# Performance work log

Hardware: AMD Instinct MI355X
Metric: run time of the kernel (lower is better)

Reference implementation:

```python
import jax, jax.numpy as jnp
import numpy as np
import math

T, B, I, H = 512, 64, 256, 512


def setup_inputs() -> dict:
    key = jax.random.key(0)
    ks = jax.random.split(key, 8)
    inp = {}
    inp["x"] = jax.random.normal(ks[0], (T, B, I), jnp.float32)
    # positive elapsed-time intervals per step/batch
    inp["time"] = jax.random.uniform(ks[1], (T, B), jnp.float32, 0.0, 2.0)
    def wn(k, shape, fan_in):
        return jax.random.normal(k, shape, jnp.float32) * (1.0 / math.sqrt(fan_in))
    # forward-direction cell params
    inp["W_ih_f"] = wn(ks[2], (I, 4 * H), I)
    inp["W_hh_f"] = wn(ks[3], (H, 4 * H), H)
    inp["b_f"] = jnp.zeros((4 * H,), jnp.float32)
    inp["W_d_f"] = wn(ks[4], (H, H), H)
    inp["b_d_f"] = jnp.zeros((H,), jnp.float32)
    # backward-direction cell params
    inp["W_ih_b"] = wn(ks[5], (I, 4 * H), I)
    inp["W_hh_b"] = wn(ks[6], (H, 4 * H), H)
    inp["b_b"] = jnp.zeros((4 * H,), jnp.float32)
    inp["W_d_b"] = wn(ks[7], (H, H), H)
    inp["b_d_b"] = jnp.zeros((H,), jnp.float32)
    return inp


def _run_direction(x, t, W_ih, W_hh, b, W_d, b_d):
    """Time-aware LSTM scan over leading axis. x: [T,B,I], t: [T,B]."""
    Bz = x.shape[1]
    Hh = W_hh.shape[0]
    E = jnp.float32(math.e)

    def step(carry, xt_tt):
        h, c = carry
        xt, tt = xt_tt  # [B,I], [B]
        # TLSTM-style time decay of short-term memory
        c_s = jnp.tanh(c @ W_d + b_d)                 # [B,H]
        c_s_hat = c_s / jnp.log(E + tt[:, None])      # decayed short-term
        c_adj = c - c_s + c_s_hat                     # adjusted cell memory
        gates = xt @ W_ih + h @ W_hh + b              # [B,4H]
        i, f, g, o = jnp.split(gates, 4, axis=-1)
        i = jax.nn.sigmoid(i)
        f = jax.nn.sigmoid(f)
        o = jax.nn.sigmoid(o)
        c_new = f * c_adj + i * jnp.tanh(g)
        h_new = o * jnp.tanh(c_new)
        return (h_new, c_new), h_new

    init = (jnp.zeros((Bz, Hh), x.dtype), jnp.zeros((Bz, Hh), x.dtype))
    _, ys = jax.lax.scan(step, init, (x, t))
    return ys  # [T,B,H]


def reference(x, time, W_ih_f, W_hh_f, b_f, W_d_f, b_d_f,
              W_ih_b, W_hh_b, b_b, W_d_b, b_d_b):
    out_f = _run_direction(x, time, W_ih_f, W_hh_f, b_f, W_d_f, b_d_f)
    # reverse direction: flip time axis, scan, flip outputs back
    out_b = _run_direction(x[::-1], time[::-1], W_ih_b, W_hh_b, b_b, W_d_b, b_d_b)[::-1]
    return jnp.concatenate([out_f, out_b], axis=-1)  # [T,B,2H]
```

## Files before the change

kernel.cpp:

```cpp
#include <hip/hip_runtime.h>
#include <cstdint>

#define T_DIM 512
#define B_DIM 64
#define I_DIM 256
#define H_DIM 512

typedef _Float16 f16x8 __attribute__((ext_vector_type(8)));
typedef float f32x4  __attribute__((ext_vector_type(4)));
typedef unsigned int u32x4 __attribute__((ext_vector_type(4)));

union H8U { f16x8 v; u32x4 u; };

#define WS_FLAGS   0u
#define WS_STATE   8192u
#define GRP_U32    16384u
#define WS_XPK     (8192u + 8u*65536u)
#define XPK_U32    (512u*4u*8u*64u*4u)
#define WS_NEED_MIN WS_XPK
#define WS_NEED_XPK (WS_XPK + XPK_U32*4u)

__device__ __forceinline__ unsigned short f2h(float f) {
  union { _Float16 h; unsigned short u; } c; c.h = (_Float16)f; return c.u;
}
__device__ __forceinline__ float sigm(float v) { return 1.0f / (1.0f + __expf(-v)); }
__device__ __forceinline__ float tanh_f(float v) {
  float e = __expf(2.0f * fabsf(v));
  float r = 1.0f - 2.0f / (e + 1.0f);
  return copysignf(r, v);
}

__device__ __forceinline__ void st_u32(unsigned* p, unsigned v) {
  asm volatile("global_store_dword %0, %1, off sc0 sc1" :: "v"(p), "v"(v) : "memory");
}
__device__ __forceinline__ unsigned ld_u32(const unsigned* p) {
  unsigned v;
  asm volatile("global_load_dword %0, %1, off sc0 sc1\n\ts_waitcnt vmcnt(0)"
               : "=v"(v) : "v"(p) : "memory");
  return v;
}

__global__ void __launch_bounds__(256) init_ws_kernel(unsigned* ws) {
  unsigned nf = WS_STATE / 4u;
  unsigned n = WS_XPK / 4u;
  for (unsigned i = blockIdx.x * 256u + threadIdx.x; i < n; i += gridDim.x * 256u)
    __hip_atomic_store(&ws[i], (i < nf) ? 0u : 5u, __ATOMIC_RELAXED, __HIP_MEMORY_SCOPE_AGENT);
}

__global__ void __launch_bounds__(256) xpack_kernel(const float* __restrict__ x,
                                                    unsigned* __restrict__ xpk) {
  size_t idx = (size_t)blockIdx.x * 256 + threadIdx.x;
  int l = (int)(idx & 63);
  size_t kt = (idx >> 6) & 7, mt = (idx >> 9) & 3, t = idx >> 11;
  const float* xp = x + ((t * 64) + mt * 16 + (size_t)(l & 15)) * 256 + kt * 32 + (size_t)(l >> 4) * 8;
  f32x4 a = *(const f32x4*)xp, b = *(const f32x4*)(xp + 4);
  float v[8] = {a[0], a[1], a[2], a[3], b[0], b[1], b[2], b[3]};
  u32x4 pk;
  #pragma unroll
  for (int i = 0; i < 4; ++i)
    pk[i] = (unsigned)f2h(v[2 * i]) | ((unsigned)f2h(v[2 * i + 1]) << 16);
  *(u32x4*)(xpk + idx * 4) = pk;
}

template <bool XPK>
__global__ void __launch_bounds__(256, 1) lstm_kernel(
    const float* __restrict__ x, const float* __restrict__ tim,
    const float* __restrict__ Wih_f, const float* __restrict__ Whh_f,
    const float* __restrict__ bias_f, const float* __restrict__ Wd_f,
    const float* __restrict__ bd_f,
    const float* __restrict__ Wih_b, const float* __restrict__ Whh_b,
    const float* __restrict__ bias_b, const float* __restrict__ Wd_b,
    const float* __restrict__ bd_b,
    float* __restrict__ out, char* __restrict__ wsb,
    const unsigned* __restrict__ xpk)
{
  const int tid = threadIdx.x;
  const int w   = tid >> 6;
  const int l   = tid & 63;
  const int lw  = l & 15;
  const int ko  = l >> 4;
  const int g   = blockIdx.x & 7;
  const int js  = blockIdx.x >> 3;
  const int dir = g & 1;
  const int mt  = g >> 1;
  const int b0  = mt * 16;

  const float* Wih  = dir ? Wih_b  : Wih_f;
  const float* Whh  = dir ? Whh_b  : Whh_f;
  const float* bias = dir ? bias_b : bias_f;
  const float* Wd   = dir ? Wd_b   : Wd_f;
  const float* bd   = dir ? bd_b   : bd_f;

  unsigned* flagbase = (unsigned*)(wsb + WS_FLAGS) + (size_t)g * 256;
  unsigned* state = (unsigned*)(wsb + WS_STATE) + (size_t)g * GRP_U32;

  __shared__ float red[4][5][16][34];

  f16x8 wx[4][2][2];
  f16x8 wh[4][4][2];
  f16x8 wd[4][2];
  #pragma unroll
  for (int xi = 0; xi < 2; ++xi) {
    const int krow = (w * 2 + xi) * 32 + ko * 8;
    #pragma unroll
    for (int g4 = 0; g4 < 4; ++g4) {
      #pragma unroll
      for (int ct = 0; ct < 2; ++ct) {
        const float* p = Wih + (size_t)krow * 2048 + g4 * 512 + js * 32 + ct * 16 + lw;
        #pragma unroll
        for (int i = 0; i < 8; ++i) wx[g4][xi][ct][i] = (_Float16)p[(size_t)i * 2048];
      }
    }
  }
  #pragma unroll
  for (int q = 0; q < 4; ++q) {
    const int krow = w * 128 + q * 32 + ko * 8;
    #pragma unroll
    for (int g4 = 0; g4 < 4; ++g4) {
      #pragma unroll
      for (int ct = 0; ct < 2; ++ct) {
        const float* p = Whh + (size_t)krow * 2048 + g4 * 512 + js * 32 + ct * 16 + lw;
        #pragma unroll
        for (int i = 0; i < 8; ++i) wh[g4][q][ct][i] = (_Float16)p[(size_t)i * 2048];
      }
    }
    #pragma unroll
    for (int ct = 0; ct < 2; ++ct) {
      const float* p2 = Wd + (size_t)krow * 512 + js * 32 + ct * 16 + lw;
      #pragma unroll
      for (int i = 0; i < 8; ++i) wd[q][ct][i] = (_Float16)p2[(size_t)i * 512];
    }
  }

  const int ub = tid >> 4;
  const int uj = tid & 15;
  float bs_i[2], bs_f[2], bs_g[2], bs_o[2], bs_d[2], c_reg[2];
  #pragma unroll
  for (int ct = 0; ct < 2; ++ct) {
    const int jg = js * 32 + ct * 16 + uj;
    bs_i[ct] = bias[jg];
    bs_f[ct] = bias[512 + jg];
    bs_g[ct] = bias[1024 + jg];
    bs_o[ct] = bias[1536 + jg];
    bs_d[ct] = bd[jg];
    c_reg[ct] = 0.0f;
  }

  u32x4 rr[4][2];
  u32x4 xpf0, xpf1;

#define ISSUE_KT(kt) do { \
    const unsigned* sp_ = state + (size_t)lslot * 8192 + (size_t)lw * 512 + w * 128 + (kt) * 32 + ko * 8; \
    asm volatile( \
        "global_load_dwordx4 %0, %2, off sc0 sc1\n\t" \
        "global_load_dwordx4 %1, %2, off offset:16 sc0 sc1" \
        : "=&v"(rr[kt][0]), "=&v"(rr[kt][1]) : "v"(sp_) : "memory"); \
  } while (0)

#define TAGOK(kt) __all((int)( \
    ((rr[kt][0][0] & 7u) == e3) & ((rr[kt][0][1] & 7u) == e3) & \
    ((rr[kt][0][2] & 7u) == e3) & ((rr[kt][0][3] & 7u) == e3) & \
    ((rr[kt][1][0] & 7u) == e3) & ((rr[kt][1][1] & 7u) == e3) & \
    ((rr[kt][1][2] & 7u) == e3) & ((rr[kt][1][3] & 7u) == e3)))

#define MFMA_KT(kt) do { \
    H8U hf_, cf_; \
    hf_.u[0] = __builtin_amdgcn_perm(rr[kt][0][1], rr[kt][0][0], 0x07060302u); \
    hf_.u[1] = __builtin_amdgcn_perm(rr[kt][0][3], rr[kt][0][2], 0x07060302u); \
    hf_.u[2] = __builtin_amdgcn_perm(rr[kt][1][1], rr[kt][1][0], 0x07060302u); \
    hf_.u[3] = __builtin_amdgcn_perm(rr[kt][1][3], rr[kt][1][2], 0x07060302u); \
    cf_.u[0] = __builtin_amdgcn_perm(rr[kt][0][1], rr[kt][0][0], 0x05040100u); \
    cf_.u[1] = __builtin_amdgcn_perm(rr[kt][0][3], rr[kt][0][2], 0x05040100u); \
    cf_.u[2] = __builtin_amdgcn_perm(rr[kt][1][1], rr[kt][1][0], 0x05040100u); \
    cf_.u[3] = __builtin_amdgcn_perm(rr[kt][1][3], rr[kt][1][2], 0x05040100u); \
    _Pragma("unroll") \
    for (int j = 0; j < 4; ++j) cf_.u[j] = (cf_.u[j] & 0xFFF8FFF8u) | 0x00040004u; \
    _Pragma("unroll") \
    for (int g4 = 0; g4 < 4; ++g4) { \
      _Pragma("unroll") \
      for (int ct = 0; ct < 2; ++ct) \
        ag[g4][ct] = __builtin_amdgcn_mfma_f32_16x16x32_f16(hf_.v, wh[g4][kt][ct], ag[g4][ct], 0, 0, 0); \
    } \
    _Pragma("unroll") \
    for (int ct = 0; ct < 2; ++ct) \
      ac[ct] = __builtin_amdgcn_mfma_f32_16x16x32_f16(cf_.v, wd[kt][ct], ac[ct], 0, 0, 0); \
  } while (0)

  if (XPK) {
    const int ts0 = dir ? (T_DIM - 1) : 0;
    const unsigned* xb = xpk + (((size_t)ts0 * 4 + mt) * 8 + w * 2) * 256 + (size_t)l * 4;
    asm volatile(
        "global_load_dwordx4 %0, %2, off\n\t"
        "global_load_dwordx4 %1, %3, off"
        : "=v"(xpf0), "=v"(xpf1) : "v"(xb), "v"(xb + 256) : "memory");
    asm volatile("s_waitcnt vmcnt(0)" ::: "memory");
    __builtin_amdgcn_sched_barrier(0);
  }

  for (int t = 0; t < T_DIM; ++t) {
    const int tsrc = dir ? (T_DIM - 1 - t) : t;
    const int sslot = t & 1;
    const int lslot = sslot ^ 1;

    float tt = tim[(size_t)tsrc * B_DIM + b0 + ub];

    f16x8 ax[2];
    if (XPK) {
      H8U u0, u1; u0.u = xpf0; u1.u = xpf1;
      ax[0] = u0.v; ax[1] = u1.v;
    } else {
      #pragma unroll
      for (int xi = 0; xi < 2; ++xi) {
        const float* xp = x + ((size_t)tsrc * B_DIM + b0 + lw) * I_DIM + (w * 2 + xi) * 32 + ko * 8;
        f32x4 v0 = *(const f32x4*)xp;
        f32x4 v1 = *(const f32x4*)(xp + 4);
        f16x8 vv;
        #pragma unroll
        for (int i = 0; i < 4; ++i) { vv[i] = (_Float16)v0[i]; vv[4 + i] = (_Float16)v1[i]; }
        ax[xi] = vv;
      }
    }

    if (t > 0) { ISSUE_KT(0); ISSUE_KT(1); ISSUE_KT(2); ISSUE_KT(3); }
    if (XPK) {
      const int tn = (t + 1 < T_DIM) ? (dir ? (T_DIM - 2 - t) : (t + 1)) : 0;
      const unsigned* xbn = xpk + (((size_t)tn * 4 + mt) * 8 + w * 2) * 256 + (size_t)l * 4;
      asm volatile(
          "global_load_dwordx4 %0, %2, off\n\t"
          "global_load_dwordx4 %1, %3, off"
          : "=v"(xpf0), "=v"(xpf1) : "v"(xbn), "v"(xbn + 256) : "memory");
    }

    f32x4 ag[4][2]; f32x4 ac[2];
    #pragma unroll
    for (int g4 = 0; g4 < 4; ++g4) { ag[g4][0] = (f32x4)0.0f; ag[g4][1] = (f32x4)0.0f; }
    ac[0] = (f32x4)0.0f; ac[1] = (f32x4)0.0f;
    #pragma unroll
    for (int xi = 0; xi < 2; ++xi) {
      #pragma unroll
      for (int g4 = 0; g4 < 4; ++g4) {
        #pragma unroll
        for (int ct = 0; ct < 2; ++ct)
          ag[g4][ct] = __builtin_amdgcn_mfma_f32_16x16x32_f16(ax[xi], wx[g4][xi][ct], ag[g4][ct], 0, 0, 0);
      }
    }

    if (t > 0) {
      if (l < 16) {
        const unsigned* fl = flagbase + (size_t)l * 16;
        while (ld_u32(fl) < (unsigned)t) { }
      }
      asm volatile("s_waitcnt vmcnt(0)" ::: "memory");
      __builtin_amdgcn_sched_barrier(0);

      const unsigned e3 = (((unsigned)(t - 1)) >> 1) & 7u;
      int f0 = !TAGOK(0), f1 = !TAGOK(1), f2 = !TAGOK(2), f3 = !TAGOK(3);
      while (f0 | f1 | f2 | f3) {
        if (f0) ISSUE_KT(0);
        if (f1) ISSUE_KT(1);
        if (f2) ISSUE_KT(2);
        if (f3) ISSUE_KT(3);
        asm volatile("s_waitcnt vmcnt(0)" ::: "memory");
        __builtin_amdgcn_sched_barrier(0);
        if (f0) f0 = !TAGOK(0);
        if (f1) f1 = !TAGOK(1);
        if (f2) f2 = !TAGOK(2);
        if (f3) f3 = !TAGOK(3);
      }

      MFMA_KT(0); MFMA_KT(1); MFMA_KT(2); MFMA_KT(3);
    }

    #pragma unroll
    for (int g4 = 0; g4 < 4; ++g4) {
      #pragma unroll
      for (int ct = 0; ct < 2; ++ct) {
        f32x4 s = ag[g4][ct];
        #pragma unroll
        for (int r = 0; r < 4; ++r) red[w][g4][ko * 4 + r][ct * 16 + lw] = s[r];
      }
    }
    #pragma unroll
    for (int ct = 0; ct < 2; ++ct) {
      f32x4 s = ac[ct];
      #pragma unroll
      for (int r = 0; r < 4; ++r) red[w][4][ko * 4 + r][ct * 16 + lw] = s[r];
    }
    asm volatile("s_waitcnt lgkmcnt(0)" ::: "memory");
    __builtin_amdgcn_s_barrier();

    const float dinv = 1.0f / __logf(2.718281828459045f + tt);
    const unsigned ptag = (((unsigned)t) >> 1) & 7u;
    float h_keep[2];
    #pragma unroll
    for (int ct = 0; ct < 2; ++ct) {
      const int cj = ct * 16 + uj;
      float gi = red[0][0][ub][cj] + red[1][0][ub][cj] + red[2][0][ub][cj] + red[3][0][ub][cj] + bs_i[ct];
      float gf = red[0][1][ub][cj] + red[1][1][ub][cj] + red[2][1][ub][cj] + red[3][1][ub][cj] + bs_f[ct];
      float gg = red[0][2][ub][cj] + red[1][2][ub][cj] + red[2][2][ub][cj] + red[3][2][ub][cj] + bs_g[ct];
      float go = red[0][3][ub][cj] + red[1][3][ub][cj] + red[2][3][ub][cj] + red[3][3][ub][cj] + bs_o[ct];
      float csv = red[0][4][ub][cj] + red[1][4][ub][cj] + red[2][4][ub][cj] + red[3][4][ub][cj] + bs_d[ct];

      float c_s = tanh_f(csv);
      float c_adj = c_reg[ct] - c_s + c_s * dinv;
      float iv = sigm(gi);
      float fv = sigm(gf);
      float ov = sigm(go);
      float gv = tanh_f(gg);
      float c_new = fv * c_adj + iv * gv;
      float h_new = ov * tanh_f(c_new);
      c_reg[ct] = c_new;
      h_keep[ct] = h_new;

      const int jglob = js * 32 + cj;
      unsigned ch = ((unsigned)f2h(c_new) & 0xFFF8u) | ptag;
      unsigned val = ((unsigned)f2h(h_new) << 16) | ch;
      st_u32(state + (size_t)sslot * 8192 + (size_t)ub * 512 + jglob, val);
    }

    asm volatile("s_waitcnt vmcnt(0)" ::: "memory");
    __syncthreads();
    if (tid == 0) st_u32(flagbase + (size_t)js * 16, (unsigned)(t + 1));
    #pragma unroll
    for (int ct = 0; ct < 2; ++ct)
      out[((size_t)tsrc * B_DIM + b0 + ub) * 1024 + dir * 512 + js * 32 + ct * 16 + uj] = h_keep[ct];
  }
#undef ISSUE_KT
#undef TAGOK
#undef MFMA_KT
}

extern "C" void kernel_launch(void* const* d_in, const int* in_sizes, int n_in,
                              void* d_out, int out_size, void* d_ws, size_t ws_size,
                              hipStream_t stream) {
  (void)in_sizes; (void)n_in; (void)out_size;
  if (ws_size < (size_t)WS_NEED_MIN) return;
  const bool use_xpk = ws_size >= (size_t)WS_NEED_XPK;

  const float* x     = (const float*)d_in[0];
  const float* tim   = (const float*)d_in[1];
  const float* Wih_f = (const float*)d_in[2];
  const float* Whh_f = (const float*)d_in[3];
  const float* b_f   = (const float*)d_in[4];
  const float* Wd_f  = (const float*)d_in[5];
  const float* bd_f  = (const float*)d_in[6];
  const float* Wih_b = (const float*)d_in[7];
  const float* Whh_b = (const float*)d_in[8];
  const float* b_b   = (const float*)d_in[9];
  const float* Wd_b  = (const float*)d_in[10];
  const float* bd_b  = (const float*)d_in[11];
  float* out = (float*)d_out;
  char* ws = (char*)d_ws;
  unsigned* xpk = (unsigned*)(ws + WS_XPK);

  hipLaunchKernelGGL(init_ws_kernel, dim3(64), dim3(256), 0, stream, (unsigned*)ws);
  if (use_xpk) {
    hipLaunchKernelGGL(xpack_kernel, dim3(4096), dim3(256), 0, stream, x, xpk);
    hipLaunchKernelGGL((lstm_kernel<true>), dim3(128), dim3(256), 0, stream,
                       x, tim, Wih_f, Whh_f, b_f, Wd_f, bd_f,
                       Wih_b, Whh_b, b_b, Wd_b, bd_b, out, ws, xpk);
  } else {
    hipLaunchKernelGGL((lstm_kernel<false>), dim3(128), dim3(256), 0, stream,
                       x, tim, Wih_f, Whh_f, b_f, Wd_f, bd_f,
                       Wih_b, Whh_b, b_b, Wd_b, bd_b, out, ws, (const unsigned*)nullptr);
  }
}
```

Measured before the change: 1.895 ms.

## Drop per-step flag handshake and rely on tagged state polling only

Removes the per-group progress flags (flag store after a vmcnt wait plus __syncthreads, and the spin on peer flags) and synchronizes only through the tag bits embedded in each packed h/c state word. Consumers now issue the state loads and re-poll until every tag matches, then run the recurrent MFMAs. The x prefetch and the end-of-step barrier move to new positions. This cuts one global round trip and a full block sync from every timestep, at the cost of more polling traffic on state words and correctness that depends entirely on the 3-bit tag scheme.

After: 1.884 ms. Within noise of the previous version (-0.6%).

```diff
diff --git a/kernel.cpp b/kernel.cpp
--- a/kernel.cpp
+++ b/kernel.cpp
@@ -12,10 +12,9 @@
 
 union H8U { f16x8 v; u32x4 u; };
 
-#define WS_FLAGS   0u
-#define WS_STATE   8192u
+#define WS_STATE   0u
 #define GRP_U32    16384u
-#define WS_XPK     (8192u + 8u*65536u)
+#define WS_XPK     (8u*65536u)
 #define XPK_U32    (512u*4u*8u*64u*4u)
 #define WS_NEED_MIN WS_XPK
 #define WS_NEED_XPK (WS_XPK + XPK_U32*4u)
@@ -33,18 +32,11 @@
 __device__ __forceinline__ void st_u32(unsigned* p, unsigned v) {
   asm volatile("global_store_dword %0, %1, off sc0 sc1" :: "v"(p), "v"(v) : "memory");
 }
-__device__ __forceinline__ unsigned ld_u32(const unsigned* p) {
-  unsigned v;
-  asm volatile("global_load_dword %0, %1, off sc0 sc1\n\ts_waitcnt vmcnt(0)"
-               : "=v"(v) : "v"(p) : "memory");
-  return v;
-}
 
 __global__ void __launch_bounds__(256) init_ws_kernel(unsigned* ws) {
-  unsigned nf = WS_STATE / 4u;
-  unsigned n = WS_XPK / 4u;
+  unsigned n = (8u * 65536u) / 4u;
   for (unsigned i = blockIdx.x * 256u + threadIdx.x; i < n; i += gridDim.x * 256u)
-    __hip_atomic_store(&ws[i], (i < nf) ? 0u : 5u, __ATOMIC_RELAXED, __HIP_MEMORY_SCOPE_AGENT);
+    __hip_atomic_store(&ws[i], 5u, __ATOMIC_RELAXED, __HIP_MEMORY_SCOPE_AGENT);
 }
 
 __global__ void __launch_bounds__(256) xpack_kernel(const float* __restrict__ x,
@@ -91,7 +83,6 @@
   const float* Wd   = dir ? Wd_b   : Wd_f;
   const float* bd   = dir ? bd_b   : bd_f;
 
-  unsigned* flagbase = (unsigned*)(wsb + WS_FLAGS) + (size_t)g * 256;
   unsigned* state = (unsigned*)(wsb + WS_STATE) + (size_t)g * GRP_U32;
 
   __shared__ float red[4][5][16][34];
@@ -193,14 +184,15 @@
         "global_load_dwordx4 %0, %2, off\n\t"
         "global_load_dwordx4 %1, %3, off"
         : "=v"(xpf0), "=v"(xpf1) : "v"(xb), "v"(xb + 256) : "memory");
-    asm volatile("s_waitcnt vmcnt(0)" ::: "memory");
-    __builtin_amdgcn_sched_barrier(0);
   }
 
   for (int t = 0; t < T_DIM; ++t) {
     const int tsrc = dir ? (T_DIM - 1 - t) : t;
     const int sslot = t & 1;
     const int lslot = sslot ^ 1;
+
+    asm volatile("s_waitcnt vmcnt(0)" ::: "memory");
+    __builtin_amdgcn_sched_barrier(0);
 
     float tt = tim[(size_t)tsrc * B_DIM + b0 + ub];
 
@@ -221,16 +213,6 @@
       }
     }
 
-    if (t > 0) { ISSUE_KT(0); ISSUE_KT(1); ISSUE_KT(2); ISSUE_KT(3); }
-    if (XPK) {
-      const int tn = (t + 1 < T_DIM) ? (dir ? (T_DIM - 2 - t) : (t + 1)) : 0;
-      const unsigned* xbn = xpk + (((size_t)tn * 4 + mt) * 8 + w * 2) * 256 + (size_t)l * 4;
-      asm volatile(
-          "global_load_dwordx4 %0, %2, off\n\t"
-          "global_load_dwordx4 %1, %3, off"
-          : "=v"(xpf0), "=v"(xpf1) : "v"(xbn), "v"(xbn + 256) : "memory");
-    }
-
     f32x4 ag[4][2]; f32x4 ac[2];
     #pragma unroll
     for (int g4 = 0; g4 < 4; ++g4) { ag[g4][0] = (f32x4)0.0f; ag[g4][1] = (f32x4)0.0f; }
@@ -246,29 +228,38 @@
     }
 
     if (t > 0) {
-      if (l < 16) {
-        const unsigned* fl = flagbase + (size_t)l * 16;
-        while (ld_u32(fl) < (unsigned)t) { }
-      }
-      asm volatile("s_waitcnt vmcnt(0)" ::: "memory");
-      __builtin_amdgcn_sched_barrier(0);
-
+      ISSUE_KT(0); ISSUE_KT(1); ISSUE_KT(2); ISSUE_KT(3);
+      if (XPK) {
+        const int tn = (t + 1 < T_DIM) ? (dir ? (T_DIM - 2 - t) : (t + 1)) : 0;
+        const unsigned* xbn = xpk + (((size_t)tn * 4 + mt) * 8 + w * 2) * 256 + (size_t)l * 4;
+        asm volatile(
+            "global_load_dwordx4 %0, %2, off\n\t"
+            "global_load_dwordx4 %1, %3, off"
+            : "=v"(xpf0), "=v"(xpf1) : "v"(xbn), "v"(xbn + 256) : "memory");
+      }
       const unsigned e3 = (((unsigned)(t - 1)) >> 1) & 7u;
-      int f0 = !TAGOK(0), f1 = !TAGOK(1), f2 = !TAGOK(2), f3 = !TAGOK(3);
-      while (f0 | f1 | f2 | f3) {
-        if (f0) ISSUE_KT(0);
-        if (f1) ISSUE_KT(1);
-        if (f2) ISSUE_KT(2);
-        if (f3) ISSUE_KT(3);
+      int f0 = 1, f1 = 1, f2 = 1, f3 = 1;
+      for (;;) {
         asm volatile("s_waitcnt vmcnt(0)" ::: "memory");
         __builtin_amdgcn_sched_barrier(0);
         if (f0) f0 = !TAGOK(0);
         if (f1) f1 = !TAGOK(1);
         if (f2) f2 = !TAGOK(2);
         if (f3) f3 = !TAGOK(3);
-      }
-
+        if (!(f0 | f1 | f2 | f3)) break;
+        if (f0) ISSUE_KT(0);
+        if (f1) ISSUE_KT(1);
+        if (f2) ISSUE_KT(2);
+        if (f3) ISSUE_KT(3);
+      }
       MFMA_KT(0); MFMA_KT(1); MFMA_KT(2); MFMA_KT(3);
+    } else if (XPK) {
+      const int tn = dir ? (T_DIM - 2) : 1;
+      const unsigned* xbn = xpk + (((size_t)tn * 4 + mt) * 8 + w * 2) * 256 + (size_t)l * 4;
+      asm volatile(
+          "global_load_dwordx4 %0, %2, off\n\t"
+          "global_load_dwordx4 %1, %3, off"
+          : "=v"(xpf0), "=v"(xpf1) : "v"(xbn), "v"(xbn + 256) : "memory");
     }
 
     #pragma unroll
@@ -318,12 +309,11 @@
       st_u32(state + (size_t)sslot * 8192 + (size_t)ub * 512 + jglob, val);
     }
 
-    asm volatile("s_waitcnt vmcnt(0)" ::: "memory");
-    __syncthreads();
-    if (tid == 0) st_u32(flagbase + (size_t)js * 16, (unsigned)(t + 1));
     #pragma unroll
     for (int ct = 0; ct < 2; ++ct)
       out[((size_t)tsrc * B_DIM + b0 + ub) * 1024 + dir * 512 + js * 32 + ct * 16 + uj] = h_keep[ct];
+
+    __builtin_amdgcn_s_barrier();
   }
 #undef ISSUE_KT
 #undef TAGOK
```
